# Performance work log

Hardware: AMD Instinct MI355X
Metric: run time of the kernel (lower is better)

The kernel has to match this reference:

```python
import jax, jax.numpy as jnp
import numpy as np

INPUT_SIZE = 1024  # enc_dim + dec_dim after concat
ENC_DIM = 512
DEC_DIM = 512
INNER_DIM = 512
VOCAB = 2048


def setup_inputs() -> dict:
    key = jax.random.key(0)
    k1, k2, k3, k4, k5, k6 = jax.random.split(key, 6)
    B, T, U = 4, 256, 128
    enc_state = jax.random.normal(k1, (B, T, ENC_DIM), dtype=jnp.float32)
    dec_state = jax.random.normal(k2, (B, U, DEC_DIM), dtype=jnp.float32)
    # forward_layer: Linear(input_size, inner_dim); stored as [in, out] for jax
    s1 = 1.0 / np.sqrt(INPUT_SIZE)
    W1 = jax.random.uniform(k3, (INPUT_SIZE, INNER_DIM), jnp.float32, -s1, s1)
    b1 = jax.random.uniform(k4, (INNER_DIM,), jnp.float32, -s1, s1)
    s2 = 1.0 / np.sqrt(INNER_DIM)
    W2 = jax.random.uniform(k5, (INNER_DIM, VOCAB), jnp.float32, -s2, s2)
    b2 = jax.random.uniform(k6, (VOCAB,), jnp.float32, -s2, s2)
    return {"enc_state": enc_state, "dec_state": dec_state,
            "W1": W1, "b1": b1, "W2": W2, "b2": b2}


def reference(enc_state, dec_state, W1, b1, W2, b2):
    # JointNet: concat(enc_repeat, dec_repeat) @ W1 + b1 -> tanh -> @ W2 + b2.
    # Since W1 acts on the concat axis, split it: concat @ W1 == enc @ W1_e + dec @ W1_d
    # (mathematically identical, avoids materializing the [B,T,U,2D] concat tensor).
    W1_enc = W1[:ENC_DIM]   # [D_enc, inner]
    W1_dec = W1[ENC_DIM:]   # [D_dec, inner]
    enc_proj = jnp.einsum('btd,dh->bth', enc_state, W1_enc)  # [B,T,H]
    dec_proj = jnp.einsum('bud,dh->buh', dec_state, W1_dec)  # [B,U,H]
    h = jnp.tanh(enc_proj[:, :, None, :] + dec_proj[:, None, :, :] + b1)  # [B,T,U,H]
    logits = jnp.einsum('btuh,hv->btuv', h, W2) + b2  # [B,T,U,V]
    return logits
```

## Files before the change

kernel.cpp:

```cpp
#include <hip/hip_runtime.h>
#include <hip/hip_bf16.h>


typedef __attribute__((ext_vector_type(4))) float f32x4;
typedef __attribute__((ext_vector_type(8))) __bf16 bf16x8;
typedef __attribute__((ext_vector_type(8))) unsigned short u16x8;

__device__ __forceinline__ float bf2f(unsigned short u) {
  unsigned int x = ((unsigned int)u) << 16;
  return __builtin_bit_cast(float, x);
}
__device__ __forceinline__ unsigned short f2bf(float f) {
  unsigned int x = __builtin_bit_cast(unsigned int, f);
  x += 0x7fff + ((x >> 16) & 1);
  return (unsigned short)(x >> 16);
}
__device__ __forceinline__ float tanh_fast(float x) {
  float e = __expf(2.0f * x);
  return 1.0f - 2.0f * __builtin_amdgcn_rcpf(e + 1.0f);
}

typedef __attribute__((address_space(3))) unsigned int lds_u32;
typedef const __attribute__((address_space(1))) unsigned int glb_u32;
__device__ __forceinline__ void gl16(const void* g, void* l) {
  __builtin_amdgcn_global_load_lds((glb_u32*)g, (lds_u32*)l, 16, 0, 0);
}

#define BAR __builtin_amdgcn_s_barrier()
#define LGKM0 asm volatile("s_waitcnt lgkmcnt(0)" ::: "memory")
#define VMCNT(n) asm volatile("s_waitcnt vmcnt(" #n ")" ::: "memory")
#define MEMPIN asm volatile("" ::: "memory")

__global__ __launch_bounds__(512) void proj8_kernel(
    const float* __restrict__ enc, const float* __restrict__ dec,
    const float* __restrict__ W1, const float* __restrict__ b1,
    float* __restrict__ enc_proj, unsigned short* __restrict__ decb) {
  __shared__ float xs[8][512];
  const int bid = blockIdx.x;
  const bool isenc = bid < 128;
  const int rows0 = (isenc ? bid : bid - 128) * 8;
  const float* src = (isenc ? enc : dec) + (size_t)rows0 * 512;
  const int tid = threadIdx.x;
#pragma unroll
  for (int j = 0; j < 2; ++j) {
    int v = j * 512 + tid;
    int row = v >> 7;
    int c4 = (v & 127) << 2;
    *(f32x4*)&xs[row][c4] = *(const f32x4*)&src[(size_t)row * 512 + c4];
  }
  __syncthreads();
  const int h = tid;
  const float* wp = W1 + (isenc ? 0 : (size_t)512 * 512) + h;
  float acc[8];
  float init = isenc ? 0.f : b1[h];
#pragma unroll
  for (int r = 0; r < 8; ++r) acc[r] = init;
#pragma unroll 4
  for (int k = 0; k < 512; ++k) {
    float wv = wp[(size_t)k * 512];
#pragma unroll
    for (int r = 0; r < 8; ++r) acc[r] = fmaf(xs[r][k], wv, acc[r]);
  }
  if (isenc) {
#pragma unroll
    for (int r = 0; r < 8; ++r) enc_proj[(size_t)(rows0 + r) * 512 + h] = acc[r];
  } else {
#pragma unroll
    for (int r = 0; r < 8; ++r) decb[(size_t)(rows0 + r) * 512 + h] = f2bf(acc[r]);
  }
}

__global__ __launch_bounds__(256) void w2t_kernel(const float* __restrict__ W2,
                                                  unsigned short* __restrict__ W2t) {
  __shared__ unsigned short tile[32][33];
  int bn = blockIdx.x;
  int bk = blockIdx.y;
  int tx = threadIdx.x & 31;
  int ty = threadIdx.x >> 5;
#pragma unroll
  for (int i = 0; i < 32; i += 8)
    tile[ty + i][tx] = f2bf(W2[(size_t)(bk * 32 + ty + i) * 2048 + bn * 32 + tx]);
  __syncthreads();
#pragma unroll
  for (int i = 0; i < 32; i += 8)
    W2t[(size_t)(bn * 32 + ty + i) * 512 + bk * 32 + tx] = tile[tx][ty + i];
}

__global__ __launch_bounds__(256) void h_kernel(
    const float* __restrict__ encp, const unsigned short* __restrict__ decb,
    unsigned short* __restrict__ Hout) {
  int gid = blockIdx.x * 256 + threadIdx.x;
  int m = gid >> 6;
  int hc = (gid & 63) << 3;
  int bt = m >> 7;
  int bu = ((m >> 15) << 7) | (m & 127);
  u16x8 dv = *(const u16x8*)(decb + (size_t)bu * 512 + hc);
  f32x4 e0 = *(const f32x4*)(encp + (size_t)bt * 512 + hc);
  f32x4 e1 = *(const f32x4*)(encp + (size_t)bt * 512 + hc + 4);
  u16x8 hv;
#pragma unroll
  for (int j = 0; j < 4; ++j) hv[j] = f2bf(tanh_fast(bf2f(dv[j]) + e0[j]));
#pragma unroll
  for (int j = 0; j < 4; ++j) hv[4 + j] = f2bf(tanh_fast(bf2f(dv[4 + j]) + e1[j]));
  *(u16x8*)(Hout + (size_t)m * 512 + hc) = hv;
}


__global__ __launch_bounds__(512, 4) void gemm32_kernel(
    const unsigned short* __restrict__ H,
    const unsigned short* __restrict__ W2t,
    const float* __restrict__ b2,
    float* __restrict__ out) {
  __shared__ __align__(1024) char smem[73728];

  const int bid = blockIdx.x;
  const int wg = (bid & 7) * 1024 + (bid >> 3);
  const int my = wg >> 4;
  const int ny = wg & 15;

  const int tid = threadIdx.x;
  const int lane = tid & 63;
  const int w = tid >> 6;
  const int wm = w >> 1;
  const int wn = w & 1;
  const int fr = lane & 15;
  const int fq = lane >> 4;

  const char* ha = (const char*)(H + (size_t)my * 256 * 512);
  const char* wb = (const char*)(W2t + (size_t)ny * 128 * 512);

  size_t srcA[2], srcB;
#pragma unroll
  for (int p = 0; p < 2; ++p) {
    int d = p * 8192 + w * 1024 + lane * 16;
    int r = d >> 6;
    int c = (d >> 4) & 3;
    srcA[p] = (size_t)r * 1024 + (size_t)((c ^ (r & 3)) << 4);
  }
  {
    int d = w * 1024 + lane * 16;
    int r = d >> 6;
    int c = (d >> 4) & 3;
    srcB = (size_t)r * 1024 + (size_t)((c ^ (r & 3)) << 4);
  }

  const int swz = (fq ^ (fr & 3)) << 4;
  const int ldsA = (wm * 64 + fr) * 64 + swz;
  const int ldsB = 16384 + (wn * 64 + fr) * 64 + swz;

  f32x4 acc[4][4];
#pragma unroll
  for (int i = 0; i < 4; ++i)
#pragma unroll
    for (int j = 0; j < 4; ++j) acc[i][j] = (f32x4){0.f, 0.f, 0.f, 0.f};

#define STAGE(tt, slot)                                         \
  do {                                                          \
    char* sl = smem + (slot)*24576;                             \
    gl16(ha + srcA[0] + (tt)*64, sl + w * 1024);                \
    gl16(ha + srcA[1] + (tt)*64, sl + 8192 + w * 1024);         \
    gl16(wb + srcB + (tt)*64, sl + 16384 + w * 1024);           \
  } while (0)

  STAGE(0, 0);
  STAGE(1, 1);

#pragma unroll
  for (int t = 0; t < 16; ++t) {
    if (t < 15) { VMCNT(3); } else { VMCNT(0); }
    BAR; MEMPIN;
    const char* As = smem + (t % 3) * 24576;
    bf16x8 a4[4], b4[4];
#pragma unroll
    for (int mi = 0; mi < 4; ++mi) a4[mi] = *(const bf16x8*)(As + ldsA + mi * 1024);
#pragma unroll
    for (int ni = 0; ni < 4; ++ni) b4[ni] = *(const bf16x8*)(As + ldsB + ni * 1024);
    if (t + 2 < 16) STAGE(t + 2, (t + 2) % 3);
    LGKM0;
    __builtin_amdgcn_s_setprio(1);
#pragma unroll
    for (int mi = 0; mi < 4; ++mi)
#pragma unroll
      for (int ni = 0; ni < 4; ++ni)
        acc[mi][ni] = __builtin_amdgcn_mfma_f32_16x16x32_bf16(
            a4[mi], b4[ni], acc[mi][ni], 0, 0, 0);
    __builtin_amdgcn_s_setprio(0);
  }
  BAR; MEMPIN;

  float* lslice = (float*)(smem + w * 4352);
  const size_t orow0 = (size_t)my * 256 + wm * 64;
  const int ncol0 = ny * 128 + wn * 64;
  float bv[4];
#pragma unroll
  for (int ni = 0; ni < 4; ++ni) bv[ni] = b2[ncol0 + ni * 16 + fr];

  const int rrow = lane >> 4;
  const int rcol = (lane & 15) * 4;
#pragma unroll
  for (int mi = 0; mi < 4; ++mi) {
#pragma unroll
    for (int ni = 0; ni < 4; ++ni)
#pragma unroll
      for (int r = 0; r < 4; ++r)
        lslice[(fq * 4 + r) * 68 + ni * 16 + fr] = acc[mi][ni][r] + bv[ni];
#pragma unroll
    for (int j = 0; j < 4; ++j) {
      int row = j * 4 + rrow;
      f32x4 v = *(const f32x4*)&lslice[row * 68 + rcol];
      __builtin_nontemporal_store(
          v, (f32x4*)&out[(orow0 + mi * 16 + row) * 2048 + ncol0 + rcol]);
    }
  }
#undef STAGE
}

extern "C" void kernel_launch(void* const* d_in, const int* in_sizes, int n_in,
                              void* d_out, int out_size, void* d_ws, size_t ws_size,
                              hipStream_t stream) {
  const float* enc = (const float*)d_in[0];
  const float* dec = (const float*)d_in[1];
  const float* W1  = (const float*)d_in[2];
  const float* b1  = (const float*)d_in[3];
  const float* W2  = (const float*)d_in[4];
  const float* b2  = (const float*)d_in[5];
  float* out = (float*)d_out;

  char* ws = (char*)d_ws;
  float* enc_proj = (float*)ws;
  unsigned short* decb = (unsigned short*)(ws + (2u << 20));
  unsigned short* W2t  = (unsigned short*)(ws + (2u << 20) + (512u << 10));
  unsigned short* Hbuf = (unsigned short*)(ws + (8u << 20));

  proj8_kernel<<<192, 512, 0, stream>>>(enc, dec, W1, b1, enc_proj, decb);
  w2t_kernel<<<dim3(64, 16), 256, 0, stream>>>(W2, W2t);
  h_kernel<<<32768, 256, 0, stream>>>(enc_proj, decb, Hbuf);
  gemm32_kernel<<<8192, 512, 0, stream>>>(Hbuf, W2t, b2, out);
}
```

Measured before the change: 406.1 us.

## Make GEMM persistent and overlap epilogue stores with next tile's MFMA

Replaces the 8192-block GEMM launch with 256 persistent blocks, each walking 32 consecutive M tiles for a fixed N tile, with the 3-slot async load pipeline continuing across tile boundaries. The previous tile's accumulators are saved (with bias) and written out through a separate LDS slice, interleaved with the next tile's MFMA iterations. This is meant to hide epilogue store latency and the pipeline prologue/drain at each tile boundary. In exchange it doubles the accumulator register count, lowers occupancy to 2 blocks per CU, and uses more LDS.

```diff
diff --git a/kernel.cpp b/kernel.cpp
--- a/kernel.cpp
+++ b/kernel.cpp
@@ -106,17 +106,18 @@
 }
 
 
-__global__ __launch_bounds__(512, 4) void gemm32_kernel(
+__global__ __launch_bounds__(512, 2) void gemmp_kernel(
     const unsigned short* __restrict__ H,
     const unsigned short* __restrict__ W2t,
     const float* __restrict__ b2,
     float* __restrict__ out) {
-  __shared__ __align__(1024) char smem[73728];
+  __shared__ __align__(1024) char smem[108544];
 
   const int bid = blockIdx.x;
-  const int wg = (bid & 7) * 1024 + (bid >> 3);
-  const int my = wg >> 4;
-  const int ny = wg & 15;
+  const int xcd = bid & 7;
+  const int slt = bid >> 3;
+  const int ny = slt & 15;
+  const int mybase = xcd * 64 + (slt >> 4) * 32;
 
   const int tid = threadIdx.x;
   const int lane = tid & 63;
@@ -126,9 +127,6 @@
   const int fr = lane & 15;
   const int fq = lane >> 4;
 
-  const char* ha = (const char*)(H + (size_t)my * 256 * 512);
-  const char* wb = (const char*)(W2t + (size_t)ny * 128 * 512);
-
   size_t srcA[2], srcB;
 #pragma unroll
   for (int p = 0; p < 2; ++p) {
@@ -148,71 +146,118 @@
   const int ldsA = (wm * 64 + fr) * 64 + swz;
   const int ldsB = 16384 + (wn * 64 + fr) * 64 + swz;
 
-  f32x4 acc[4][4];
+  const char* wbase = (const char*)W2t + (size_t)ny * 128 * 1024;
+  const int ncol0 = ny * 128 + wn * 64;
+
+  float bv[4];
+#pragma unroll
+  for (int ni = 0; ni < 4; ++ni) bv[ni] = b2[ncol0 + ni * 16 + fr];
+
+  f32x4 acc[4][4], sacc[4][4];
 #pragma unroll
   for (int i = 0; i < 4; ++i)
 #pragma unroll
     for (int j = 0; j < 4; ++j) acc[i][j] = (f32x4){0.f, 0.f, 0.f, 0.f};
 
-#define STAGE(tt, slot)                                         \
-  do {                                                          \
-    char* sl = smem + (slot)*24576;                             \
-    gl16(ha + srcA[0] + (tt)*64, sl + w * 1024);                \
-    gl16(ha + srcA[1] + (tt)*64, sl + 8192 + w * 1024);         \
-    gl16(wb + srcB + (tt)*64, sl + 16384 + w * 1024);           \
-  } while (0)
-
-  STAGE(0, 0);
-  STAGE(1, 1);
-
-#pragma unroll
-  for (int t = 0; t < 16; ++t) {
-    if (t < 15) { VMCNT(3); } else { VMCNT(0); }
-    BAR; MEMPIN;
-    const char* As = smem + (t % 3) * 24576;
-    bf16x8 a4[4], b4[4];
-#pragma unroll
-    for (int mi = 0; mi < 4; ++mi) a4[mi] = *(const bf16x8*)(As + ldsA + mi * 1024);
-#pragma unroll
-    for (int ni = 0; ni < 4; ++ni) b4[ni] = *(const bf16x8*)(As + ldsB + ni * 1024);
-    if (t + 2 < 16) STAGE(t + 2, (t + 2) % 3);
-    LGKM0;
-    __builtin_amdgcn_s_setprio(1);
-#pragma unroll
-    for (int mi = 0; mi < 4; ++mi)
-#pragma unroll
-      for (int ni = 0; ni < 4; ++ni)
-        acc[mi][ni] = __builtin_amdgcn_mfma_f32_16x16x32_bf16(
-            a4[mi], b4[ni], acc[mi][ni], 0, 0, 0);
-    __builtin_amdgcn_s_setprio(0);
-  }
-  BAR; MEMPIN;
-
-  float* lslice = (float*)(smem + w * 4352);
-  const size_t orow0 = (size_t)my * 256 + wm * 64;
-  const int ncol0 = ny * 128 + wn * 64;
-  float bv[4];
-#pragma unroll
-  for (int ni = 0; ni < 4; ++ni) bv[ni] = b2[ncol0 + ni * 16 + fr];
-
+  float* lslice = (float*)(smem + 73728 + w * 4352);
   const int rrow = lane >> 4;
   const int rcol = (lane & 15) * 4;
-#pragma unroll
-  for (int mi = 0; mi < 4; ++mi) {
-#pragma unroll
-    for (int ni = 0; ni < 4; ++ni)
-#pragma unroll
-      for (int r = 0; r < 4; ++r)
-        lslice[(fq * 4 + r) * 68 + ni * 16 + fr] = acc[mi][ni][r] + bv[ni];
-#pragma unroll
-    for (int j = 0; j < 4; ++j) {
-      int row = j * 4 + rrow;
-      f32x4 v = *(const f32x4*)&lslice[row * 68 + rcol];
-      __builtin_nontemporal_store(
-          v, (f32x4*)&out[(orow0 + mi * 16 + row) * 2048 + ncol0 + rcol]);
+
+#define STAGEG(g)                                                        \
+  do {                                                                   \
+    int tg_ = (g) >> 4;                                                  \
+    int ks_ = (g) & 15;                                                  \
+    char* sl_ = smem + ((g) % 3) * 24576;                                \
+    const char* ha_ = (const char*)H + ((size_t)(mybase + tg_) << 18);   \
+    gl16(ha_ + srcA[0] + ks_ * 64, sl_ + w * 1024);                      \
+    gl16(ha_ + srcA[1] + ks_ * 64, sl_ + 8192 + w * 1024);               \
+    gl16(wbase + srcB + ks_ * 64, sl_ + 16384 + w * 1024);               \
+  } while (0)
+
+  STAGEG(0);
+  STAGEG(1);
+
+#pragma unroll 1
+  for (int tt = 0; tt < 32; ++tt) {
+    const bool st = tt > 0;
+    const size_t prow0 = ((size_t)(mybase + tt - 1) << 8) + wm * 64;
+#pragma unroll
+    for (int p = 0; p < 16; ++p) {
+      const int g = tt * 16 + p;
+      if (p == 15) {
+        if (tt == 31) { VMCNT(0); } else if (tt <= 1) { VMCNT(3); } else { VMCNT(4); }
+      } else {
+        if (tt <= 1) { VMCNT(3); } else { VMCNT(4); }
+      }
+      BAR; MEMPIN;
+
+      const char* As = smem + (g % 3) * 24576;
+      bf16x8 a4[4], b4[4];
+#pragma unroll
+      for (int mi = 0; mi < 4; ++mi) a4[mi] = *(const bf16x8*)(As + ldsA + mi * 1024);
+#pragma unroll
+      for (int ni = 0; ni < 4; ++ni) b4[ni] = *(const bf16x8*)(As + ldsB + ni * 1024);
+
+      if (g + 2 < 512) STAGEG(g + 2);
+      MEMPIN;
+
+      if (st && (p & 3) == 0) {
+        const int mi = p >> 2;
+#pragma unroll
+        for (int ni = 0; ni < 4; ++ni)
+#pragma unroll
+          for (int r = 0; r < 4; ++r)
+            lslice[(fq * 4 + r) * 68 + ni * 16 + fr] = sacc[mi][ni][r];
+      }
+      LGKM0;
+
+      __builtin_amdgcn_s_setprio(1);
+#pragma unroll
+      for (int mi = 0; mi < 4; ++mi)
+#pragma unroll
+        for (int ni = 0; ni < 4; ++ni)
+          acc[mi][ni] = __builtin_amdgcn_mfma_f32_16x16x32_bf16(
+              a4[mi], b4[ni], acc[mi][ni], 0, 0, 0);
+      __builtin_amdgcn_s_setprio(0);
+
+      if (st) {
+        const int mi = p >> 2;
+        const int row = (p & 3) * 4 + rrow;
+        f32x4 v = *(const f32x4*)&lslice[row * 68 + rcol];
+        __builtin_nontemporal_store(
+            v, (f32x4*)&out[(prow0 + mi * 16 + row) * 2048 + ncol0 + rcol]);
+      }
     }
-  }
-#undef STAGE
+#pragma unroll
+    for (int mi = 0; mi < 4; ++mi)
+#pragma unroll
+      for (int ni = 0; ni < 4; ++ni) {
+#pragma unroll
+        for (int r = 0; r < 4; ++r) sacc[mi][ni][r] = acc[mi][ni][r] + bv[ni];
+        acc[mi][ni] = (f32x4){0.f, 0.f, 0.f, 0.f};
+      }
+  }
+
+  {
+    const size_t prow0 = ((size_t)(mybase + 31) << 8) + wm * 64;
+#pragma unroll
+    for (int mi = 0; mi < 4; ++mi) {
+#pragma unroll
+      for (int ni = 0; ni < 4; ++ni)
+#pragma unroll
+        for (int r = 0; r < 4; ++r)
+          lslice[(fq * 4 + r) * 68 + ni * 16 + fr] = sacc[mi][ni][r];
+      LGKM0;
+#pragma unroll
+      for (int j = 0; j < 4; ++j) {
+        const int row = j * 4 + rrow;
+        f32x4 v = *(const f32x4*)&lslice[row * 68 + rcol];
+        __builtin_nontemporal_store(
+            v, (f32x4*)&out[(prow0 + mi * 16 + row) * 2048 + ncol0 + rcol]);
+      }
+    }
+  }
+#undef STAGEG
 }
 
 extern "C" void kernel_launch(void* const* d_in, const int* in_sizes, int n_in,
@@ -235,5 +280,5 @@
   proj8_kernel<<<192, 512, 0, stream>>>(enc, dec, W1, b1, enc_proj, decb);
   w2t_kernel<<<dim3(64, 16), 256, 0, stream>>>(W2, W2t);
   h_kernel<<<32768, 256, 0, stream>>>(enc_proj, decb, Hbuf);
-  gemm32_kernel<<<8192, 512, 0, stream>>>(Hbuf, W2t, b2, out);
-}
+  gemmp_kernel<<<256, 512, 0, stream>>>(Hbuf, W2t, b2, out);
+}
```

After: 436.7 us. 1.08x slower.

## Convert output GEMM to persistent row-block kernel sweeping all vocab tiles

Applied to the files above, without the earlier changes.

Replaces the 8192-block GEMM launch with 512 persistent blocks. Each block owns one 256-row strip of H and loops over all 16 vocab column tiles, keeping the load pipeline running across tile boundaries and caching b2 in LDS. The epilogue reuses a pipeline slot, handled in two halves of waves. Blocks beyond 256 sleep briefly at start to stagger them. This cuts per-block launch and prologue overhead and improves reuse of the A strip, but makes the epilogue serialize with compute and depends on how well 512 blocks fill the device.

```diff
diff --git a/kernel.cpp b/kernel.cpp
--- a/kernel.cpp
+++ b/kernel.cpp
@@ -106,17 +106,15 @@
 }
 
 
-__global__ __launch_bounds__(512, 4) void gemm32_kernel(
+__global__ __launch_bounds__(512, 4) void gemmps_kernel(
     const unsigned short* __restrict__ H,
     const unsigned short* __restrict__ W2t,
     const float* __restrict__ b2,
     float* __restrict__ out) {
-  __shared__ __align__(1024) char smem[73728];
+  __shared__ __align__(1024) char smem[81920];
 
   const int bid = blockIdx.x;
-  const int wg = (bid & 7) * 1024 + (bid >> 3);
-  const int my = wg >> 4;
-  const int ny = wg & 15;
+  const int my = bid & 511;
 
   const int tid = threadIdx.x;
   const int lane = tid & 63;
@@ -126,9 +124,6 @@
   const int fr = lane & 15;
   const int fq = lane >> 4;
 
-  const char* ha = (const char*)(H + (size_t)my * 256 * 512);
-  const char* wb = (const char*)(W2t + (size_t)ny * 128 * 512);
-
   size_t srcA[2], srcB;
 #pragma unroll
   for (int p = 0; p < 2; ++p) {
@@ -148,71 +143,138 @@
   const int ldsA = (wm * 64 + fr) * 64 + swz;
   const int ldsB = 16384 + (wn * 64 + fr) * 64 + swz;
 
+  const char* ha = (const char*)H + ((size_t)my << 18);
+  float* b2l = (float*)(smem + 73728);
+
+  {
+    f32x4 bchunk = *(const f32x4*)&b2[tid * 4];
+    *(f32x4*)&b2l[tid * 4] = bchunk;
+  }
+  __syncthreads();
+
+  if (bid >= 256) {
+    asm volatile("s_sleep 127");
+    asm volatile("s_sleep 64");
+  }
+
   f32x4 acc[4][4];
 #pragma unroll
   for (int i = 0; i < 4; ++i)
 #pragma unroll
     for (int j = 0; j < 4; ++j) acc[i][j] = (f32x4){0.f, 0.f, 0.f, 0.f};
-
-#define STAGE(tt, slot)                                         \
-  do {                                                          \
-    char* sl = smem + (slot)*24576;                             \
-    gl16(ha + srcA[0] + (tt)*64, sl + w * 1024);                \
-    gl16(ha + srcA[1] + (tt)*64, sl + 8192 + w * 1024);         \
-    gl16(wb + srcB + (tt)*64, sl + 16384 + w * 1024);           \
-  } while (0)
-
-  STAGE(0, 0);
-  STAGE(1, 1);
-
-#pragma unroll
-  for (int t = 0; t < 16; ++t) {
-    if (t < 15) { VMCNT(3); } else { VMCNT(0); }
-    BAR; MEMPIN;
-    const char* As = smem + (t % 3) * 24576;
-    bf16x8 a4[4], b4[4];
-#pragma unroll
-    for (int mi = 0; mi < 4; ++mi) a4[mi] = *(const bf16x8*)(As + ldsA + mi * 1024);
-#pragma unroll
-    for (int ni = 0; ni < 4; ++ni) b4[ni] = *(const bf16x8*)(As + ldsB + ni * 1024);
-    if (t + 2 < 16) STAGE(t + 2, (t + 2) % 3);
-    LGKM0;
-    __builtin_amdgcn_s_setprio(1);
-#pragma unroll
-    for (int mi = 0; mi < 4; ++mi)
-#pragma unroll
-      for (int ni = 0; ni < 4; ++ni)
-        acc[mi][ni] = __builtin_amdgcn_mfma_f32_16x16x32_bf16(
-            a4[mi], b4[ni], acc[mi][ni], 0, 0, 0);
-    __builtin_amdgcn_s_setprio(0);
-  }
-  BAR; MEMPIN;
-
-  float* lslice = (float*)(smem + w * 4352);
-  const size_t orow0 = (size_t)my * 256 + wm * 64;
-  const int ncol0 = ny * 128 + wn * 64;
-  float bv[4];
-#pragma unroll
-  for (int ni = 0; ni < 4; ++ni) bv[ni] = b2[ncol0 + ni * 16 + fr];
 
   const int rrow = lane >> 4;
   const int rcol = (lane & 15) * 4;
-#pragma unroll
-  for (int mi = 0; mi < 4; ++mi) {
-#pragma unroll
-    for (int ni = 0; ni < 4; ++ni)
-#pragma unroll
-      for (int r = 0; r < 4; ++r)
-        lslice[(fq * 4 + r) * 68 + ni * 16 + fr] = acc[mi][ni][r] + bv[ni];
-#pragma unroll
-    for (int j = 0; j < 4; ++j) {
-      int row = j * 4 + rrow;
-      f32x4 v = *(const f32x4*)&lslice[row * 68 + rcol];
-      __builtin_nontemporal_store(
-          v, (f32x4*)&out[(orow0 + mi * 16 + row) * 2048 + ncol0 + rcol]);
+
+#define STAGEG2(tg_, ks_, sl_)                                           \
+  do {                                                                   \
+    char* slp_ = smem + (sl_)*24576;                                     \
+    const char* wb_ = (const char*)W2t + ((size_t)(tg_) << 17);          \
+    gl16(ha + srcA[0] + (ks_)*64, slp_ + w * 1024);                      \
+    gl16(ha + srcA[1] + (ks_)*64, slp_ + 8192 + w * 1024);               \
+    gl16(wb_ + srcB + (ks_)*64, slp_ + 16384 + w * 1024);                \
+  } while (0)
+
+  STAGEG2(0, 0, 0);
+  STAGEG2(0, 1, 1);
+
+  int sl = 0;
+  int sp = 2;
+
+#pragma unroll 1
+  for (int tt = 0; tt < 16; ++tt) {
+#pragma unroll
+    for (int p = 0; p < 16; ++p) {
+      if (tt == 15 && p == 15) {
+        VMCNT(0);
+      } else if (p < 2) {
+        if (tt > 0) { VMCNT(19); } else { VMCNT(3); }
+      } else {
+        VMCNT(3);
+      }
+      BAR; MEMPIN;
+
+      const char* As = smem + sl * 24576;
+      bf16x8 a4[4], b4[4];
+#pragma unroll
+      for (int mi = 0; mi < 4; ++mi) a4[mi] = *(const bf16x8*)(As + ldsA + mi * 1024);
+#pragma unroll
+      for (int ni = 0; ni < 4; ++ni) b4[ni] = *(const bf16x8*)(As + ldsB + ni * 1024);
+
+      if (!(tt == 15 && p >= 14)) {
+        const int ks2 = (p + 2) & 15;
+        const int tg2 = tt + ((p + 2) >> 4);
+        STAGEG2(tg2, ks2, sp);
+      }
+      LGKM0;
+
+      __builtin_amdgcn_s_setprio(1);
+#pragma unroll
+      for (int mi = 0; mi < 4; ++mi)
+#pragma unroll
+        for (int ni = 0; ni < 4; ++ni)
+          acc[mi][ni] = __builtin_amdgcn_mfma_f32_16x16x32_bf16(
+              a4[mi], b4[ni], acc[mi][ni], 0, 0, 0);
+      __builtin_amdgcn_s_setprio(0);
+
+      const int slc = sl;
+      sl = (sl == 2) ? 0 : sl + 1;
+      sp = (sp == 2) ? 0 : sp + 1;
+
+      if (p == 15) {
+        BAR; MEMPIN;
+        const size_t rbase = ((size_t)my << 8) + wm * 64;
+        const int ncol0 = tt * 128 + wn * 64;
+        float bvv[4];
+#pragma unroll
+        for (int ni = 0; ni < 4; ++ni) bvv[ni] = b2l[ncol0 + ni * 16 + fr];
+
+        char* slotp = smem + slc * 24576;
+        if (w < 4) {
+          float* ls = (float*)slotp + w * 1088;
+#pragma unroll
+          for (int mi = 0; mi < 4; ++mi) {
+#pragma unroll
+            for (int ni = 0; ni < 4; ++ni)
+#pragma unroll
+              for (int r = 0; r < 4; ++r)
+                ls[(fq * 4 + r) * 68 + ni * 16 + fr] = acc[mi][ni][r] + bvv[ni];
+#pragma unroll
+            for (int j = 0; j < 4; ++j) {
+              const int row = j * 4 + rrow;
+              f32x4 v = *(const f32x4*)&ls[row * 68 + rcol];
+              __builtin_nontemporal_store(
+                  v, (f32x4*)&out[(rbase + mi * 16 + row) * 2048 + ncol0 + rcol]);
+            }
+          }
+        }
+        BAR; MEMPIN;
+        if (w >= 4) {
+          float* ls = (float*)slotp + (w - 4) * 1088;
+#pragma unroll
+          for (int mi = 0; mi < 4; ++mi) {
+#pragma unroll
+            for (int ni = 0; ni < 4; ++ni)
+#pragma unroll
+              for (int r = 0; r < 4; ++r)
+                ls[(fq * 4 + r) * 68 + ni * 16 + fr] = acc[mi][ni][r] + bvv[ni];
+#pragma unroll
+            for (int j = 0; j < 4; ++j) {
+              const int row = j * 4 + rrow;
+              f32x4 v = *(const f32x4*)&ls[row * 68 + rcol];
+              __builtin_nontemporal_store(
+                  v, (f32x4*)&out[(rbase + mi * 16 + row) * 2048 + ncol0 + rcol]);
+            }
+          }
+        }
+#pragma unroll
+        for (int i = 0; i < 4; ++i)
+#pragma unroll
+          for (int j = 0; j < 4; ++j) acc[i][j] = (f32x4){0.f, 0.f, 0.f, 0.f};
+      }
     }
   }
-#undef STAGE
+#undef STAGEG2
 }
 
 extern "C" void kernel_launch(void* const* d_in, const int* in_sizes, int n_in,
@@ -235,5 +297,5 @@
   proj8_kernel<<<192, 512, 0, stream>>>(enc, dec, W1, b1, enc_proj, decb);
   w2t_kernel<<<dim3(64, 16), 256, 0, stream>>>(W2, W2t);
   h_kernel<<<32768, 256, 0, stream>>>(enc_proj, decb, Hbuf);
-  gemm32_kernel<<<8192, 512, 0, stream>>>(Hbuf, W2t, b2, out);
-}
+  gemmps_kernel<<<512, 512, 0, stream>>>(Hbuf, W2t, b2, out);
+}
```

After: 774.8 us. +90.8%, slower.

## Make GEMM persistent and warp-specialized with a dedicated store wave

Applied to the files above, without the earlier changes.

Replaces the 8192-block GEMM with 512 persistent blocks. Each block runs 16 output tiles back to back with a continuous load pipeline across tile boundaries. A ninth wave does the output stores: compute waves stage finished accumulators plus bias into LDS chunks, and the store wave streams them to global memory while the next tile's MFMAs run. The LDS swizzle pattern also changes. This targets launch/tail overhead and overlaps the large fp32 output write with compute, at the cost of more LDS, lower occupancy (2 blocks), and tricky barrier and vmcnt coordination.

```diff
diff --git a/kernel.cpp b/kernel.cpp
--- a/kernel.cpp
+++ b/kernel.cpp
@@ -106,28 +106,26 @@
 }
 
 
-__global__ __launch_bounds__(512, 4) void gemm32_kernel(
+__global__ __launch_bounds__(576, 2) void gemmws_kernel(
     const unsigned short* __restrict__ H,
     const unsigned short* __restrict__ W2t,
     const float* __restrict__ b2,
     float* __restrict__ out) {
-  __shared__ __align__(1024) char smem[73728];
+  __shared__ __align__(1024) char smem[107520];
 
   const int bid = blockIdx.x;
-  const int wg = (bid & 7) * 1024 + (bid >> 3);
-  const int my = wg >> 4;
-  const int ny = wg & 15;
+  const int base = (bid & 7) * 1024 + (bid >> 3);
+  const int my0 = base >> 4;
+  const int ny = base & 15;
 
   const int tid = threadIdx.x;
   const int lane = tid & 63;
   const int w = tid >> 6;
-  const int wm = w >> 1;
+  const bool compute = (w < 8);
+  const int wm = (w >> 1) & 3;
   const int wn = w & 1;
   const int fr = lane & 15;
   const int fq = lane >> 4;
-
-  const char* ha = (const char*)(H + (size_t)my * 256 * 512);
-  const char* wb = (const char*)(W2t + (size_t)ny * 128 * 512);
 
   size_t srcA[2], srcB;
 #pragma unroll
@@ -135,84 +133,126 @@
     int d = p * 8192 + w * 1024 + lane * 16;
     int r = d >> 6;
     int c = (d >> 4) & 3;
-    srcA[p] = (size_t)r * 1024 + (size_t)((c ^ (r & 3)) << 4);
+    srcA[p] = (size_t)r * 1024 + (size_t)((c ^ ((r >> 1) & 3)) << 4);
   }
   {
     int d = w * 1024 + lane * 16;
     int r = d >> 6;
     int c = (d >> 4) & 3;
-    srcB = (size_t)r * 1024 + (size_t)((c ^ (r & 3)) << 4);
-  }
-
-  const int swz = (fq ^ (fr & 3)) << 4;
+    srcB = (size_t)r * 1024 + (size_t)((c ^ ((r >> 1) & 3)) << 4);
+  }
+  const int swz = (fq ^ ((fr >> 1) & 3)) << 4;
   const int ldsA = (wm * 64 + fr) * 64 + swz;
   const int ldsB = 16384 + (wn * 64 + fr) * 64 + swz;
 
-  f32x4 acc[4][4];
+  const int C0 = ny * 128;
+  float bv[4];
+  if (compute) {
+#pragma unroll
+    for (int ni = 0; ni < 4; ++ni) bv[ni] = b2[C0 + wn * 64 + ni * 16 + fr];
+  }
+
+  f32x4 acc[4][4], sacc[4][4];
 #pragma unroll
   for (int i = 0; i < 4; ++i)
 #pragma unroll
-    for (int j = 0; j < 4; ++j) acc[i][j] = (f32x4){0.f, 0.f, 0.f, 0.f};
-
-#define STAGE(tt, slot)                                         \
-  do {                                                          \
-    char* sl = smem + (slot)*24576;                             \
-    gl16(ha + srcA[0] + (tt)*64, sl + w * 1024);                \
-    gl16(ha + srcA[1] + (tt)*64, sl + 8192 + w * 1024);         \
-    gl16(wb + srcB + (tt)*64, sl + 16384 + w * 1024);           \
+    for (int j = 0; j < 4; ++j) {
+      acc[i][j] = (f32x4){0.f, 0.f, 0.f, 0.f};
+      sacc[i][j] = (f32x4){0.f, 0.f, 0.f, 0.f};
+    }
+
+#define STAGEW(gg)                                                            \
+  do {                                                                        \
+    const int gg_ = (gg);                                                     \
+    char* sl_ = smem + (gg_ % 3) * 24576;                                     \
+    const char* ha_ =                                                         \
+        (const char*)H + ((size_t)(my0 + 4 * (gg_ >> 4)) << 18);              \
+    const char* wb_ = (const char*)W2t + ((size_t)ny << 17);                  \
+    const size_t ko_ = (size_t)(gg_ & 15) * 64;                               \
+    gl16(ha_ + srcA[0] + ko_, sl_ + w * 1024);                                \
+    gl16(ha_ + srcA[1] + ko_, sl_ + 8192 + w * 1024);                         \
+    gl16(wb_ + srcB + ko_, sl_ + 16384 + w * 1024);                           \
   } while (0)
 
-  STAGE(0, 0);
-  STAGE(1, 1);
-
-#pragma unroll
-  for (int t = 0; t < 16; ++t) {
-    if (t < 15) { VMCNT(3); } else { VMCNT(0); }
+  if (compute) {
+    STAGEW(0);
+    STAGEW(1);
+  }
+
+#pragma unroll 1
+  for (int g = 0; g < 274; ++g) {
+    if (compute) {
+      if (g <= 254) { VMCNT(3); }
+      else if (g == 255) { VMCNT(0); }
+    } else {
+      VMCNT(40);
+    }
     BAR; MEMPIN;
-    const char* As = smem + (t % 3) * 24576;
-    bf16x8 a4[4], b4[4];
-#pragma unroll
-    for (int mi = 0; mi < 4; ++mi) a4[mi] = *(const bf16x8*)(As + ldsA + mi * 1024);
-#pragma unroll
-    for (int ni = 0; ni < 4; ++ni) b4[ni] = *(const bf16x8*)(As + ldsB + ni * 1024);
-    if (t + 2 < 16) STAGE(t + 2, (t + 2) % 3);
-    LGKM0;
-    __builtin_amdgcn_s_setprio(1);
-#pragma unroll
-    for (int mi = 0; mi < 4; ++mi)
-#pragma unroll
-      for (int ni = 0; ni < 4; ++ni)
-        acc[mi][ni] = __builtin_amdgcn_mfma_f32_16x16x32_bf16(
-            a4[mi], b4[ni], acc[mi][ni], 0, 0, 0);
-    __builtin_amdgcn_s_setprio(0);
-  }
-  BAR; MEMPIN;
-
-  float* lslice = (float*)(smem + w * 4352);
-  const size_t orow0 = (size_t)my * 256 + wm * 64;
-  const int ncol0 = ny * 128 + wn * 64;
-  float bv[4];
-#pragma unroll
-  for (int ni = 0; ni < 4; ++ni) bv[ni] = b2[ncol0 + ni * 16 + fr];
-
-  const int rrow = lane >> 4;
-  const int rcol = (lane & 15) * 4;
-#pragma unroll
-  for (int mi = 0; mi < 4; ++mi) {
-#pragma unroll
-    for (int ni = 0; ni < 4; ++ni)
-#pragma unroll
-      for (int r = 0; r < 4; ++r)
-        lslice[(fq * 4 + r) * 68 + ni * 16 + fr] = acc[mi][ni][r] + bv[ni];
-#pragma unroll
-    for (int j = 0; j < 4; ++j) {
-      int row = j * 4 + rrow;
-      f32x4 v = *(const f32x4*)&lslice[row * 68 + rcol];
-      __builtin_nontemporal_store(
-          v, (f32x4*)&out[(orow0 + mi * 16 + row) * 2048 + ncol0 + rcol]);
+
+    if (compute) {
+      bf16x8 a4[4], b4[4];
+      if (g < 256) {
+        const char* As = smem + (g % 3) * 24576;
+#pragma unroll
+        for (int mi = 0; mi < 4; ++mi) a4[mi] = *(const bf16x8*)(As + ldsA + mi * 1024);
+#pragma unroll
+        for (int ni = 0; ni < 4; ++ni) b4[ni] = *(const bf16x8*)(As + ldsB + ni * 1024);
+        if (g + 2 < 256) STAGEW(g + 2);
+      }
+      {
+        const int ct = g >> 4;
+        if (ct >= 1 && ct <= 16 && ((g >> 2) & 3) == wm) {
+          const int mi = g & 3;
+          float* cb = (float*)(smem + 73728 + (g & 3) * 8448);
+#pragma unroll
+          for (int ni = 0; ni < 4; ++ni)
+#pragma unroll
+            for (int rr = 0; rr < 4; ++rr)
+              cb[(fq * 4 + rr) * 132 + wn * 64 + ni * 16 + fr] = sacc[mi][ni][rr];
+        }
+      }
+      LGKM0;
+      if (g < 256) {
+        __builtin_amdgcn_s_setprio(1);
+#pragma unroll
+        for (int mi = 0; mi < 4; ++mi)
+#pragma unroll
+          for (int ni = 0; ni < 4; ++ni)
+            acc[mi][ni] = __builtin_amdgcn_mfma_f32_16x16x32_bf16(
+                a4[mi], b4[ni], acc[mi][ni], 0, 0, 0);
+        __builtin_amdgcn_s_setprio(0);
+        if ((g & 15) == 15) {
+#pragma unroll
+          for (int mi = 0; mi < 4; ++mi)
+#pragma unroll
+            for (int ni = 0; ni < 4; ++ni) {
+#pragma unroll
+              for (int rr = 0; rr < 4; ++rr)
+                sacc[mi][ni][rr] = acc[mi][ni][rr] + bv[ni];
+              acc[mi][ni] = (f32x4){0.f, 0.f, 0.f, 0.f};
+            }
+        }
+      }
+    } else {
+      const int gc = g - 2;
+      if (gc >= 16 && gc <= 271) {
+        const float* cb = (const float*)(smem + 73728 + (gc & 3) * 8448);
+        const int T = (gc >> 4) - 1;
+        const int c = gc & 15;
+        const size_t R0 = (size_t)(my0 + 4 * T) * 256 + c * 16;
+        const int ric0 = lane >> 5;
+        const int colf = (lane & 31) * 4;
+#pragma unroll
+        for (int j = 0; j < 8; ++j) {
+          const int ric = j * 2 + ric0;
+          f32x4 v = *(const f32x4*)&cb[ric * 132 + colf];
+          __builtin_nontemporal_store(
+              v, (f32x4*)&out[(R0 + ric) * 2048 + C0 + colf]);
+        }
+      }
     }
   }
-#undef STAGE
+#undef STAGEW
 }
 
 extern "C" void kernel_launch(void* const* d_in, const int* in_sizes, int n_in,
@@ -235,5 +275,5 @@
   proj8_kernel<<<192, 512, 0, stream>>>(enc, dec, W1, b1, enc_proj, decb);
   w2t_kernel<<<dim3(64, 16), 256, 0, stream>>>(W2, W2t);
   h_kernel<<<32768, 256, 0, stream>>>(enc_proj, decb, Hbuf);
-  gemm32_kernel<<<8192, 512, 0, stream>>>(Hbuf, W2t, b2, out);
-}
+  gemmws_kernel<<<512, 576, 0, stream>>>(Hbuf, W2t, b2, out);
+}
```

Result: slower. 796.5 us (+96.2%).
